# Kernel optimization log

Hardware: AMD Instinct MI355X
Metric: run time of the kernel (lower is better)

## Reference

```python
import jax, jax.numpy as jnp
import numpy as np

B, N, D, DK = 8, 2048, 1024, 64
GAMMA = 0.001

def setup_inputs() -> dict:
    key = jax.random.key(0)
    ks = jax.random.split(key, 6)
    x = jax.random.normal(ks[0], (B, N, D), dtype=jnp.float32)
    # nn.Linear weights are [out_features, in_features]; init std=gamma,
    # except fc1/fc2 (modules 4,5) which get std=1e-12 in the original.
    Wq = GAMMA * jax.random.normal(ks[1], (DK, D), dtype=jnp.float32)
    Wk = GAMMA * jax.random.normal(ks[2], (DK, D), dtype=jnp.float32)
    Wv = GAMMA * jax.random.normal(ks[3], (D, D), dtype=jnp.float32)
    W1 = 1e-12 * jax.random.normal(ks[4], (DK, D), dtype=jnp.float32)
    W2 = 1e-12 * jax.random.normal(ks[5], (D, DK), dtype=jnp.float32)
    return {"x": x, "Wq": Wq, "Wk": Wk, "Wv": Wv, "W1": W1, "W2": W2}

def reference(x, Wq, Wk, Wv, W1, W2):
    # Q,K: [B,N,DK]; V: [B,N,D]
    Q = jnp.einsum('bnd,kd->bnk', x, Wq)
    K = jnp.einsum('bnd,kd->bnk', x, Wk)
    V = jnp.einsum('bnd,ed->bne', x, Wv)
    # Linear (non-softmax) attention: (Q @ K^T) @ V
    scores = jnp.einsum('bnk,bmk->bnm', Q, K)      # [B,N,N]
    attention = jnp.einsum('bnm,bme->bne', scores, V)  # [B,N,D]
    x_skip = x + attention
    fc = jnp.einsum('bnd,kd->bnk', x_skip, W1)     # [B,N,DK]
    out = jnp.einsum('bnk,dk->bnd', fc, W2)        # [B,N,D]
    return out
```

## Files before the change

kernel.cpp:

```cpp
#include <hip/hip_runtime.h>

typedef __attribute__((ext_vector_type(8))) __bf16 bf16x8;
typedef __attribute__((ext_vector_type(4))) float f32x4;
typedef unsigned short u16;

#define MFMA16(a, b, c) __builtin_amdgcn_mfma_f32_16x16x32_bf16(a, b, c, 0, 0, 0)

__device__ __forceinline__ u16 f2bf(float f) {
    unsigned u = __float_as_uint(f);
    unsigned r = ((u >> 16) & 1u) + 0x7fffu;
    return (u16)((u + r) >> 16);
}
__device__ __forceinline__ float bf2f(u16 h) {
    return __uint_as_float(((unsigned)h) << 16);
}
__device__ __forceinline__ bf16x8 frag(const u16* base, int rtile, int lane, int kofs) {
    return *(const bf16x8*)(base + (rtile + (lane & 15)) * 72 + kofs + (lane >> 4) * 8);
}

__global__ __launch_bounds__(256) void qkf_kernel(
    const float* __restrict__ x, const float* __restrict__ Wq,
    const float* __restrict__ Wk, const float* __restrict__ W1,
    float* __restrict__ Qp, float* __restrict__ Kp, float* __restrict__ fcp)
{
    __shared__ __align__(16) u16 SM[6 * 4608];
    u16* Xh  = SM;
    u16* Xl  = SM + 4608;
    u16* Wqh = SM + 2 * 4608;
    u16* Wkh = SM + 3 * 4608;
    u16* W1h = SM + 4 * 4608;
    u16* W1l = SM + 5 * 4608;

    const int tid  = threadIdx.x;
    const int lane = tid & 63;
    const int wv   = tid >> 6;
    const int r0   = wv * 16;
    const long row0 = (long)blockIdx.x * 64;
    const int kb   = blockIdx.y * 512;
    const long sOf = (long)blockIdx.y * 1048576;

    const f32x4 zero = {0.f, 0.f, 0.f, 0.f};
    f32x4 qa[4], ka[4], fa[4];
#pragma unroll
    for (int i = 0; i < 4; ++i) { qa[i] = zero; ka[i] = zero; fa[i] = zero; }

    const int sr = tid >> 4;
    const int sk = (tid & 15) * 4;

    float4 xv[4], qv[4], kv[4], w1v[4];
#define QKF_LOAD(K0)                                                          \
    {                                                                         \
        _Pragma("unroll")                                                     \
        for (int i = 0; i < 4; ++i) {                                         \
            int r = sr + i * 16;                                              \
            xv[i]  = *(const float4*)(x  + (row0 + r) * 1024 + (K0) + sk);    \
            qv[i]  = *(const float4*)(Wq + (long)r * 1024 + (K0) + sk);       \
            kv[i]  = *(const float4*)(Wk + (long)r * 1024 + (K0) + sk);       \
            w1v[i] = *(const float4*)(W1 + (long)r * 1024 + (K0) + sk);       \
        }                                                                     \
    }

    QKF_LOAD(kb)
    for (int ch = 0; ch < 8; ++ch) {
        if (ch) __syncthreads();
#pragma unroll
        for (int i = 0; i < 4; ++i) {
            int r = sr + i * 16;
            ushort4 h, l;
            h.x = f2bf(xv[i].x); l.x = f2bf(xv[i].x - bf2f(h.x));
            h.y = f2bf(xv[i].y); l.y = f2bf(xv[i].y - bf2f(h.y));
            h.z = f2bf(xv[i].z); l.z = f2bf(xv[i].z - bf2f(h.z));
            h.w = f2bf(xv[i].w); l.w = f2bf(xv[i].w - bf2f(h.w));
            *(ushort4*)&Xh[r * 72 + sk] = h;
            *(ushort4*)&Xl[r * 72 + sk] = l;
            ushort4 hq;
            hq.x = f2bf(qv[i].x); hq.y = f2bf(qv[i].y);
            hq.z = f2bf(qv[i].z); hq.w = f2bf(qv[i].w);
            *(ushort4*)&Wqh[r * 72 + sk] = hq;
            ushort4 hk;
            hk.x = f2bf(kv[i].x); hk.y = f2bf(kv[i].y);
            hk.z = f2bf(kv[i].z); hk.w = f2bf(kv[i].w);
            *(ushort4*)&Wkh[r * 72 + sk] = hk;
            ushort4 hw, lw;
            hw.x = f2bf(w1v[i].x); lw.x = f2bf(w1v[i].x - bf2f(hw.x));
            hw.y = f2bf(w1v[i].y); lw.y = f2bf(w1v[i].y - bf2f(hw.y));
            hw.z = f2bf(w1v[i].z); lw.z = f2bf(w1v[i].z - bf2f(hw.z));
            hw.w = f2bf(w1v[i].w); lw.w = f2bf(w1v[i].w - bf2f(hw.w));
            *(ushort4*)&W1h[r * 72 + sk] = hw;
            *(ushort4*)&W1l[r * 72 + sk] = lw;
        }
        __syncthreads();
        if (ch < 7) QKF_LOAD(kb + (ch + 1) * 64)
#pragma unroll
        for (int kk = 0; kk < 64; kk += 32) {
            bf16x8 ah = frag(Xh, r0, lane, kk);
            bf16x8 al = frag(Xl, r0, lane, kk);
#pragma unroll
            for (int ct = 0; ct < 4; ++ct) {
                qa[ct] = MFMA16(ah, frag(Wqh, ct * 16, lane, kk), qa[ct]);
                ka[ct] = MFMA16(ah, frag(Wkh, ct * 16, lane, kk), ka[ct]);
                bf16x8 bh = frag(W1h, ct * 16, lane, kk);
                fa[ct] = MFMA16(ah, bh, fa[ct]);
                fa[ct] = MFMA16(al, bh, fa[ct]);
                fa[ct] = MFMA16(ah, frag(W1l, ct * 16, lane, kk), fa[ct]);
            }
        }
    }
#undef QKF_LOAD

    const int rr = r0 + (lane >> 4) * 4;
    const int cc = lane & 15;
#pragma unroll
    for (int ct = 0; ct < 4; ++ct)
#pragma unroll
        for (int g = 0; g < 4; ++g) {
            long o = sOf + (row0 + rr + g) * 64 + ct * 16 + cc;
            Qp[o]  = qa[ct][g];
            Kp[o]  = ka[ct][g];
            fcp[o] = fa[ct][g];
        }
}

__global__ __launch_bounds__(256) void s_kernel(
    const float* __restrict__ Kp, const float* __restrict__ x,
    float* __restrict__ Sp)
{
    __shared__ __align__(16) u16 Kt[64 * 72];
    __shared__ __align__(16) u16 Xt[64 * 72];

    const int tid = threadIdx.x, lane = tid & 63, wv = tid >> 6;
    const int dt = blockIdx.x, ks = blockIdx.y, b = blockIdx.z;
    const int n0 = ks * 256, d0 = dt * 64;

    const float* Kq = Kp + ((long)b * 2048 + n0) * 64;
    const float* xp = x  + ((long)b * 2048 + n0) * 1024 + d0;

    const f32x4 zero = {0.f, 0.f, 0.f, 0.f};
    f32x4 acc[4];
#pragma unroll
    for (int i = 0; i < 4; ++i) acc[i] = zero;

    float4 kf[4], xv[4];
#define SK_LOAD(NB)                                                           \
    {                                                                         \
        _Pragma("unroll")                                                     \
        for (int i = 0; i < 4; ++i) {                                         \
            float4 a = *(const float4*)(Kq + (long)((NB) + lane) * 64 + wv * 16 + i * 4); \
            float4 c = *(const float4*)(Kq + 1048576 + (long)((NB) + lane) * 64 + wv * 16 + i * 4); \
            kf[i].x = a.x + c.x; kf[i].y = a.y + c.y;                         \
            kf[i].z = a.z + c.z; kf[i].w = a.w + c.w;                         \
            xv[i] = *(const float4*)(xp + (long)((NB) + lane) * 1024 + wv * 16 + i * 4); \
        }                                                                     \
    }

    SK_LOAD(0)
    for (int ch = 0; ch < 4; ++ch) {
        if (ch) __syncthreads();
#pragma unroll
        for (int i = 0; i < 4; ++i) {
            Kt[(wv * 16 + i * 4 + 0) * 72 + lane] = f2bf(kf[i].x);
            Kt[(wv * 16 + i * 4 + 1) * 72 + lane] = f2bf(kf[i].y);
            Kt[(wv * 16 + i * 4 + 2) * 72 + lane] = f2bf(kf[i].z);
            Kt[(wv * 16 + i * 4 + 3) * 72 + lane] = f2bf(kf[i].w);
            Xt[(wv * 16 + i * 4 + 0) * 72 + lane] = f2bf(xv[i].x);
            Xt[(wv * 16 + i * 4 + 1) * 72 + lane] = f2bf(xv[i].y);
            Xt[(wv * 16 + i * 4 + 2) * 72 + lane] = f2bf(xv[i].z);
            Xt[(wv * 16 + i * 4 + 3) * 72 + lane] = f2bf(xv[i].w);
        }
        __syncthreads();
        if (ch < 3) SK_LOAD((ch + 1) * 64)
#pragma unroll
        for (int kk = 0; kk < 64; kk += 32) {
            bf16x8 a = frag(Kt, wv * 16, lane, kk);
#pragma unroll
            for (int ct = 0; ct < 4; ++ct)
                acc[ct] = MFMA16(a, frag(Xt, ct * 16, lane, kk), acc[ct]);
        }
    }
#undef SK_LOAD

    float* C = Sp + ((long)ks * 8 + b) * 65536 + d0;
    const int rr = wv * 16 + (lane >> 4) * 4;
    const int cc = lane & 15;
#pragma unroll
    for (int ct = 0; ct < 4; ++ct)
#pragma unroll
        for (int g = 0; g < 4; ++g)
            C[(long)(rr + g) * 1024 + ct * 16 + cc] = acc[ct][g];
}

template <int AMODE, int BMODE, bool SPLIT, int ASLAB, int BSLAB, int CSLAB>
__global__ __launch_bounds__(256) void mm_nt(
    const void* __restrict__ Ap, int lda, long bsA, long slabA,
    const void* __restrict__ Bp, int ldb, long bsB, long slabB,
    float* __restrict__ Cp, int ldc, long bsC, long splitC,
    const float* __restrict__ Cin, long slabCin,
    int Kred, int nksplit)
{
    __shared__ __align__(16) u16 SMEM[(SPLIT ? 4 : 2) * 4608];
    u16* Ah = SMEM;
    u16* Bh = SMEM + 4608;
    u16* Al = SPLIT ? SMEM + 2 * 4608 : nullptr;
    u16* Bl = SPLIT ? SMEM + 3 * 4608 : nullptr;

    const int tid = threadIdx.x, lane = tid & 63, wv = tid >> 6;
    const int bm = blockIdx.x, bn = blockIdx.y;
    const int batch = blockIdx.z / nksplit;
    const int ks = blockIdx.z % nksplit;
    const int Kper = Kred / nksplit;
    const long kOff = (long)ks * Kper;

    const int r4 = tid >> 4, k4 = (tid & 15) * 4;
    const int r8 = tid >> 3, k8 = (tid & 7) * 8;

    const f32x4 zero = {0.f, 0.f, 0.f, 0.f};
    f32x4 acc[4];
#pragma unroll
    for (int i = 0; i < 4; ++i) acc[i] = zero;

    float4 fva[4], fvb[4];
    uint4  uva[2], uvb[2];
    float  tvb[16];

#define MM_LOADA(K0)                                                          \
    if constexpr (AMODE == 0) {                                               \
        const float* A = (const float*)Ap + (long)batch * bsA                 \
                       + (long)bm * 64 * lda + (K0);                          \
        _Pragma("unroll")                                                     \
        for (int i = 0; i < 4; ++i) {                                         \
            const float* p = A + (long)(r4 + i * 16) * lda + k4;              \
            float4 v = *(const float4*)p;                                     \
            _Pragma("unroll")                                                 \
            for (int s = 1; s < ASLAB; ++s) {                                 \
                float4 w = *(const float4*)(p + (long)s * slabA);             \
                v.x += w.x; v.y += w.y; v.z += w.z; v.w += w.w;               \
            }                                                                 \
            fva[i] = v;                                                       \
        }                                                                     \
    } else {                                                                  \
        const u16* A = (const u16*)Ap + (long)batch * bsA                     \
                     + (long)bm * 64 * lda + (K0);                            \
        _Pragma("unroll")                                                     \
        for (int i = 0; i < 2; ++i)                                           \
            uva[i] = *(const uint4*)(A + (long)(r8 + i * 32) * lda + k8);     \
    }
#define MM_LOADB(K0)                                                          \
    if constexpr (BMODE == 0) {                                               \
        const float* Bq = (const float*)Bp + (long)batch * bsB                \
                        + (long)bn * 64 * ldb + (K0);                         \
        _Pragma("unroll")                                                     \
        for (int i = 0; i < 4; ++i) {                                         \
            const float* p = Bq + (long)(r4 + i * 16) * ldb + k4;             \
            float4 v = *(const float4*)p;                                     \
            _Pragma("unroll")                                                 \
            for (int s = 1; s < BSLAB; ++s) {                                 \
                float4 w = *(const float4*)(p + (long)s * slabB);             \
                v.x += w.x; v.y += w.y; v.z += w.z; v.w += w.w;               \
            }                                                                 \
            fvb[i] = v;                                                       \
        }                                                                     \
    } else if constexpr (BMODE == 1) {                                        \
        const u16* Bq = (const u16*)Bp + (long)batch * bsB                    \
                      + (long)bn * 64 * ldb + (K0);                           \
        _Pragma("unroll")                                                     \
        for (int i = 0; i < 2; ++i)                                           \
            uvb[i] = *(const uint4*)(Bq + (long)(r8 + i * 32) * ldb + k8);    \
    } else {                                                                  \
        const float* Bq = (const float*)Bp + (long)batch * bsB                \
                        + (long)(K0) * ldb + (long)bn * 64;                   \
        _Pragma("unroll")                                                     \
        for (int i = 0; i < 16; ++i)                                          \
            tvb[i] = Bq[(long)((tid >> 6) + i * 4) * ldb + (tid & 63)];       \
    }

    MM_LOADA(kOff) MM_LOADB(kOff)
    for (int k0 = 0; k0 < Kper; k0 += 64) {
        if (k0) __syncthreads();
        if constexpr (AMODE == 0) {
#pragma unroll
            for (int i = 0; i < 4; ++i) {
                int r = r4 + i * 16;
                ushort4 h;
                h.x = f2bf(fva[i].x); h.y = f2bf(fva[i].y);
                h.z = f2bf(fva[i].z); h.w = f2bf(fva[i].w);
                *(ushort4*)&Ah[r * 72 + k4] = h;
                if constexpr (SPLIT) {
                    ushort4 l;
                    l.x = f2bf(fva[i].x - bf2f(h.x)); l.y = f2bf(fva[i].y - bf2f(h.y));
                    l.z = f2bf(fva[i].z - bf2f(h.z)); l.w = f2bf(fva[i].w - bf2f(h.w));
                    *(ushort4*)&Al[r * 72 + k4] = l;
                }
            }
        } else {
#pragma unroll
            for (int i = 0; i < 2; ++i)
                *(uint4*)&Ah[(r8 + i * 32) * 72 + k8] = uva[i];
        }
        if constexpr (BMODE == 0) {
#pragma unroll
            for (int i = 0; i < 4; ++i) {
                int r = r4 + i * 16;
                ushort4 h;
                h.x = f2bf(fvb[i].x); h.y = f2bf(fvb[i].y);
                h.z = f2bf(fvb[i].z); h.w = f2bf(fvb[i].w);
                *(ushort4*)&Bh[r * 72 + k4] = h;
                if constexpr (SPLIT) {
                    ushort4 l;
                    l.x = f2bf(fvb[i].x - bf2f(h.x)); l.y = f2bf(fvb[i].y - bf2f(h.y));
                    l.z = f2bf(fvb[i].z - bf2f(h.z)); l.w = f2bf(fvb[i].w - bf2f(h.w));
                    *(ushort4*)&Bl[r * 72 + k4] = l;
                }
            }
        } else if constexpr (BMODE == 1) {
#pragma unroll
            for (int i = 0; i < 2; ++i)
                *(uint4*)&Bh[(r8 + i * 32) * 72 + k8] = uvb[i];
        } else {
#pragma unroll
            for (int i = 0; i < 16; ++i)
                Bh[(tid & 63) * 72 + (tid >> 6) + i * 4] = f2bf(tvb[i]);
        }
        __syncthreads();
        if (k0 + 64 < Kper) { MM_LOADA(kOff + k0 + 64) MM_LOADB(kOff + k0 + 64) }
#pragma unroll
        for (int kk = 0; kk < 64; kk += 32) {
            bf16x8 ah = frag(Ah, wv * 16, lane, kk);
            bf16x8 al;
            if constexpr (SPLIT) al = frag(Al, wv * 16, lane, kk);
#pragma unroll
            for (int ct = 0; ct < 4; ++ct) {
                bf16x8 bh = frag(Bh, ct * 16, lane, kk);
                acc[ct] = MFMA16(ah, bh, acc[ct]);
                if constexpr (SPLIT) {
                    acc[ct] = MFMA16(al, bh, acc[ct]);
                    acc[ct] = MFMA16(ah, frag(Bl, ct * 16, lane, kk), acc[ct]);
                }
            }
        }
    }
#undef MM_LOADA
#undef MM_LOADB

    const long coff = (long)batch * bsC + (long)bm * 64 * ldc + (long)bn * 64;
    float* C = Cp + coff + (long)ks * splitC;
    const int rr = wv * 16 + (lane >> 4) * 4;
    const int cc = lane & 15;
#pragma unroll
    for (int ct = 0; ct < 4; ++ct)
#pragma unroll
        for (int g = 0; g < 4; ++g) {
            long idx = (long)(rr + g) * ldc + ct * 16 + cc;
            float v = acc[ct][g];
            if constexpr (CSLAB > 0) {
                const float* Ci = Cin + coff + idx;
#pragma unroll
                for (int s = 0; s < CSLAB; ++s) v += Ci[(long)s * slabCin];
            }
            C[idx] = v;
        }
}

extern "C" void kernel_launch(void* const* d_in, const int* in_sizes, int n_in,
                              void* d_out, int out_size, void* d_ws, size_t ws_size,
                              hipStream_t stream)
{
    const float* x  = (const float*)d_in[0];
    const float* Wq = (const float*)d_in[1];
    const float* Wk = (const float*)d_in[2];
    const float* Wv = (const float*)d_in[3];
    const float* W1 = (const float*)d_in[4];
    const float* W2 = (const float*)d_in[5];
    float* out = (float*)d_out;

    const size_t QPB = 8388608, KPB = 8388608, FCPB = 8388608,
                 SPB = 16777216, GPB = 2097152, PBB = 2097152, FCB = 4194304;
    const size_t need = QPB + KPB + FCPB + SPB + GPB + PBB + FCB;

    float *Qp, *Kp, *fcp, *Sp, *Gp, *PBp, *fcb;
    if (ws_size >= need) {
        char* w = (char*)d_ws;
        Qp  = (float*)w;  w += QPB;
        Kp  = (float*)w;  w += KPB;
        fcp = (float*)w;  w += FCPB;
        Sp  = (float*)w;  w += SPB;
        Gp  = (float*)w;  w += GPB;
        PBp = (float*)w;  w += PBB;
        fcb = (float*)w;
    } else {
        char* o = (char*)d_out;
        Qp  = (float*)o;  o += QPB;
        Kp  = (float*)o;  o += KPB;
        fcp = (float*)o;  o += FCPB;
        Sp  = (float*)o;  o += SPB;
        Gp  = (float*)o;  o += GPB;
        PBp = (float*)o;
        fcb = (float*)d_ws;
    }

    qkf_kernel<<<dim3(256, 2), 256, 0, stream>>>(x, Wq, Wk, W1, Qp, Kp, fcp);

    s_kernel<<<dim3(16, 8, 8), 256, 0, stream>>>(Kp, x, Sp);

    mm_nt<0, 2, false, 1, 1, 0><<<dim3(1, 16, 8), 256, 0, stream>>>(
        W1, 1024, 0, 0,   Wv, 1024, 0, 0,
        Gp, 1024, 0, 65536L, nullptr, 0, 1024, 8);

    mm_nt<0, 0, false, 8, 8, 0><<<dim3(1, 1, 128), 256, 0, stream>>>(
        Gp, 1024, 0, 65536L,   Sp, 1024, 65536L, 524288L,
        PBp, 64, 4096L, 32768L, nullptr, 0, 1024, 16);

    mm_nt<0, 0, false, 2, 16, 2><<<dim3(32, 1, 8), 256, 0, stream>>>(
        Qp, 64, 131072L, 1048576L,   PBp, 64, 4096L, 32768L,
        fcb, 64, 131072L, 0, fcp, 1048576L, 64, 1);

    mm_nt<0, 0, true, 1, 1, 0><<<dim3(256, 16, 1), 256, 0, stream>>>(
        fcb, 64, 0, 0,   W2, 64, 0, 0,
        out, 1024, 0, 0, nullptr, 0, 64, 1);
}
```

Before: 207.0 us.

## Split qkf K-reduction four ways and fuse final two matmuls into one kernel

The QK/fc projection kernel now splits the D reduction into four slabs of 256 with a 32-wide K chunk. That doubles the grid and shrinks shared memory so more blocks can be resident, with a launch-bounds occupancy hint added. The last two matmuls (Q·PB plus fc residual, then the fc·W2 output projection) are fused into a single fcout kernel. It sums the split-K partials on load and keeps the fc tile in shared memory, avoiding an intermediate global buffer and a launch. The trade-off is larger partial buffers and more partial-sum reads in the downstream kernels. The mm_nt template is also trimmed of its unused modes.

```diff
diff --git a/kernel.cpp b/kernel.cpp
--- a/kernel.cpp
+++ b/kernel.cpp
@@ -17,46 +17,50 @@
 __device__ __forceinline__ bf16x8 frag(const u16* base, int rtile, int lane, int kofs) {
     return *(const bf16x8*)(base + (rtile + (lane & 15)) * 72 + kofs + (lane >> 4) * 8);
 }
-
-__global__ __launch_bounds__(256) void qkf_kernel(
+__device__ __forceinline__ bf16x8 frag40(const u16* base, int rtile, int lane) {
+    return *(const bf16x8*)(base + (rtile + (lane & 15)) * 40 + (lane >> 4) * 8);
+}
+
+__global__ __launch_bounds__(256, 4) void qkf_kernel(
     const float* __restrict__ x, const float* __restrict__ Wq,
     const float* __restrict__ Wk, const float* __restrict__ W1,
     float* __restrict__ Qp, float* __restrict__ Kp, float* __restrict__ fcp)
 {
-    __shared__ __align__(16) u16 SM[6 * 4608];
+    __shared__ __align__(16) u16 SM[6 * 2560];
     u16* Xh  = SM;
-    u16* Xl  = SM + 4608;
-    u16* Wqh = SM + 2 * 4608;
-    u16* Wkh = SM + 3 * 4608;
-    u16* W1h = SM + 4 * 4608;
-    u16* W1l = SM + 5 * 4608;
+    u16* Xl  = SM + 2560;
+    u16* Wqh = SM + 2 * 2560;
+    u16* Wkh = SM + 3 * 2560;
+    u16* W1h = SM + 4 * 2560;
+    u16* W1l = SM + 5 * 2560;
 
     const int tid  = threadIdx.x;
     const int lane = tid & 63;
     const int wv   = tid >> 6;
     const int r0   = wv * 16;
     const long row0 = (long)blockIdx.x * 64;
-    const int kb   = blockIdx.y * 512;
-    const long sOf = (long)blockIdx.y * 1048576;
+    const int ks   = blockIdx.y;
+    const int kb   = ks * 256;
+    const long sOf = (long)ks * 1048576;
 
     const f32x4 zero = {0.f, 0.f, 0.f, 0.f};
     f32x4 qa[4], ka[4], fa[4];
 #pragma unroll
     for (int i = 0; i < 4; ++i) { qa[i] = zero; ka[i] = zero; fa[i] = zero; }
 
-    const int sr = tid >> 4;
-    const int sk = (tid & 15) * 4;
-
-    float4 xv[4], qv[4], kv[4], w1v[4];
+    const int sr  = tid >> 2;
+    const int skq = (tid & 3) * 8;
+
+    float4 xv[2], qv[2], kv[2], w1v[2];
 #define QKF_LOAD(K0)                                                          \
     {                                                                         \
         _Pragma("unroll")                                                     \
-        for (int i = 0; i < 4; ++i) {                                         \
-            int r = sr + i * 16;                                              \
-            xv[i]  = *(const float4*)(x  + (row0 + r) * 1024 + (K0) + sk);    \
-            qv[i]  = *(const float4*)(Wq + (long)r * 1024 + (K0) + sk);       \
-            kv[i]  = *(const float4*)(Wk + (long)r * 1024 + (K0) + sk);       \
-            w1v[i] = *(const float4*)(W1 + (long)r * 1024 + (K0) + sk);       \
+        for (int h = 0; h < 2; ++h) {                                         \
+            int col = (K0) + skq + h * 4;                                     \
+            xv[h]  = *(const float4*)(x  + (row0 + sr) * 1024 + col);         \
+            qv[h]  = *(const float4*)(Wq + (long)sr * 1024 + col);            \
+            kv[h]  = *(const float4*)(Wk + (long)sr * 1024 + col);            \
+            w1v[h] = *(const float4*)(W1 + (long)sr * 1024 + col);            \
         }                                                                     \
     }
 
@@ -64,45 +68,44 @@
     for (int ch = 0; ch < 8; ++ch) {
         if (ch) __syncthreads();
 #pragma unroll
-        for (int i = 0; i < 4; ++i) {
-            int r = sr + i * 16;
-            ushort4 h, l;
-            h.x = f2bf(xv[i].x); l.x = f2bf(xv[i].x - bf2f(h.x));
-            h.y = f2bf(xv[i].y); l.y = f2bf(xv[i].y - bf2f(h.y));
-            h.z = f2bf(xv[i].z); l.z = f2bf(xv[i].z - bf2f(h.z));
-            h.w = f2bf(xv[i].w); l.w = f2bf(xv[i].w - bf2f(h.w));
-            *(ushort4*)&Xh[r * 72 + sk] = h;
-            *(ushort4*)&Xl[r * 72 + sk] = l;
+        for (int h = 0; h < 2; ++h) {
+            int o = sr * 40 + skq + h * 4;
+            ushort4 hx, lx;
+            hx.x = f2bf(xv[h].x); lx.x = f2bf(xv[h].x - bf2f(hx.x));
+            hx.y = f2bf(xv[h].y); lx.y = f2bf(xv[h].y - bf2f(hx.y));
+            hx.z = f2bf(xv[h].z); lx.z = f2bf(xv[h].z - bf2f(hx.z));
+            hx.w = f2bf(xv[h].w); lx.w = f2bf(xv[h].w - bf2f(hx.w));
+            *(ushort4*)&Xh[o] = hx;
+            *(ushort4*)&Xl[o] = lx;
             ushort4 hq;
-            hq.x = f2bf(qv[i].x); hq.y = f2bf(qv[i].y);
-            hq.z = f2bf(qv[i].z); hq.w = f2bf(qv[i].w);
-            *(ushort4*)&Wqh[r * 72 + sk] = hq;
+            hq.x = f2bf(qv[h].x); hq.y = f2bf(qv[h].y);
+            hq.z = f2bf(qv[h].z); hq.w = f2bf(qv[h].w);
+            *(ushort4*)&Wqh[o] = hq;
             ushort4 hk;
-            hk.x = f2bf(kv[i].x); hk.y = f2bf(kv[i].y);
-            hk.z = f2bf(kv[i].z); hk.w = f2bf(kv[i].w);
-            *(ushort4*)&Wkh[r * 72 + sk] = hk;
+            hk.x = f2bf(kv[h].x); hk.y = f2bf(kv[h].y);
+            hk.z = f2bf(kv[h].z); hk.w = f2bf(kv[h].w);
+            *(ushort4*)&Wkh[o] = hk;
             ushort4 hw, lw;
-            hw.x = f2bf(w1v[i].x); lw.x = f2bf(w1v[i].x - bf2f(hw.x));
-            hw.y = f2bf(w1v[i].y); lw.y = f2bf(w1v[i].y - bf2f(hw.y));
-            hw.z = f2bf(w1v[i].z); lw.z = f2bf(w1v[i].z - bf2f(hw.z));
-            hw.w = f2bf(w1v[i].w); lw.w = f2bf(w1v[i].w - bf2f(hw.w));
-            *(ushort4*)&W1h[r * 72 + sk] = hw;
-            *(ushort4*)&W1l[r * 72 + sk] = lw;
+            hw.x = f2bf(w1v[h].x); lw.x = f2bf(w1v[h].x - bf2f(hw.x));
+            hw.y = f2bf(w1v[h].y); lw.y = f2bf(w1v[h].y - bf2f(hw.y));
+            hw.z = f2bf(w1v[h].z); lw.z = f2bf(w1v[h].z - bf2f(hw.z));
+            hw.w = f2bf(w1v[h].w); lw.w = f2bf(w1v[h].w - bf2f(hw.w));
+            *(ushort4*)&W1h[o] = hw;
+            *(ushort4*)&W1l[o] = lw;
         }
         __syncthreads();
-        if (ch < 7) QKF_LOAD(kb + (ch + 1) * 64)
-#pragma unroll
-        for (int kk = 0; kk < 64; kk += 32) {
-            bf16x8 ah = frag(Xh, r0, lane, kk);
-            bf16x8 al = frag(Xl, r0, lane, kk);
+        if (ch < 7) QKF_LOAD(kb + (ch + 1) * 32)
+        {
+            bf16x8 ah = frag40(Xh, r0, lane);
+            bf16x8 al = frag40(Xl, r0, lane);
 #pragma unroll
             for (int ct = 0; ct < 4; ++ct) {
-                qa[ct] = MFMA16(ah, frag(Wqh, ct * 16, lane, kk), qa[ct]);
-                ka[ct] = MFMA16(ah, frag(Wkh, ct * 16, lane, kk), ka[ct]);
-                bf16x8 bh = frag(W1h, ct * 16, lane, kk);
+                qa[ct] = MFMA16(ah, frag40(Wqh, ct * 16, lane), qa[ct]);
+                ka[ct] = MFMA16(ah, frag40(Wkh, ct * 16, lane), ka[ct]);
+                bf16x8 bh = frag40(W1h, ct * 16, lane);
                 fa[ct] = MFMA16(ah, bh, fa[ct]);
                 fa[ct] = MFMA16(al, bh, fa[ct]);
-                fa[ct] = MFMA16(ah, frag(W1l, ct * 16, lane, kk), fa[ct]);
+                fa[ct] = MFMA16(ah, frag40(W1l, ct * 16, lane), fa[ct]);
             }
         }
     }
@@ -121,7 +124,7 @@
         }
 }
 
-__global__ __launch_bounds__(256) void s_kernel(
+__global__ __launch_bounds__(256, 4) void s_kernel(
     const float* __restrict__ Kp, const float* __restrict__ x,
     float* __restrict__ Sp)
 {
@@ -145,10 +148,14 @@
     {                                                                         \
         _Pragma("unroll")                                                     \
         for (int i = 0; i < 4; ++i) {                                         \
-            float4 a = *(const float4*)(Kq + (long)((NB) + lane) * 64 + wv * 16 + i * 4); \
-            float4 c = *(const float4*)(Kq + 1048576 + (long)((NB) + lane) * 64 + wv * 16 + i * 4); \
-            kf[i].x = a.x + c.x; kf[i].y = a.y + c.y;                         \
-            kf[i].z = a.z + c.z; kf[i].w = a.w + c.w;                         \
+            const float* kp0 = Kq + (long)((NB) + lane) * 64 + wv * 16 + i * 4; \
+            float4 a = *(const float4*)kp0;                                   \
+            _Pragma("unroll")                                                 \
+            for (int s = 1; s < 4; ++s) {                                     \
+                float4 c = *(const float4*)(kp0 + (long)s * 1048576);         \
+                a.x += c.x; a.y += c.y; a.z += c.z; a.w += c.w;               \
+            }                                                                 \
+            kf[i] = a;                                                        \
             xv[i] = *(const float4*)(xp + (long)((NB) + lane) * 1024 + wv * 16 + i * 4); \
         }                                                                     \
     }
@@ -189,19 +196,16 @@
             C[(long)(rr + g) * 1024 + ct * 16 + cc] = acc[ct][g];
 }
 
-template <int AMODE, int BMODE, bool SPLIT, int ASLAB, int BSLAB, int CSLAB>
+template <int AMODE, int BMODE, int ASLAB, int BSLAB>
 __global__ __launch_bounds__(256) void mm_nt(
     const void* __restrict__ Ap, int lda, long bsA, long slabA,
     const void* __restrict__ Bp, int ldb, long bsB, long slabB,
     float* __restrict__ Cp, int ldc, long bsC, long splitC,
-    const float* __restrict__ Cin, long slabCin,
     int Kred, int nksplit)
 {
-    __shared__ __align__(16) u16 SMEM[(SPLIT ? 4 : 2) * 4608];
+    __shared__ __align__(16) u16 SMEM[2 * 4608];
     u16* Ah = SMEM;
     u16* Bh = SMEM + 4608;
-    u16* Al = SPLIT ? SMEM + 2 * 4608 : nullptr;
-    u16* Bl = SPLIT ? SMEM + 3 * 4608 : nullptr;
 
     const int tid = threadIdx.x, lane = tid & 63, wv = tid >> 6;
     const int bm = blockIdx.x, bn = blockIdx.y;
@@ -211,7 +215,6 @@
     const long kOff = (long)ks * Kper;
 
     const int r4 = tid >> 4, k4 = (tid & 15) * 4;
-    const int r8 = tid >> 3, k8 = (tid & 7) * 8;
 
     const f32x4 zero = {0.f, 0.f, 0.f, 0.f};
     f32x4 acc[4];
@@ -219,11 +222,10 @@
     for (int i = 0; i < 4; ++i) acc[i] = zero;
 
     float4 fva[4], fvb[4];
-    uint4  uva[2], uvb[2];
     float  tvb[16];
 
 #define MM_LOADA(K0)                                                          \
-    if constexpr (AMODE == 0) {                                               \
+    {                                                                         \
         const float* A = (const float*)Ap + (long)batch * bsA                 \
                        + (long)bm * 64 * lda + (K0);                          \
         _Pragma("unroll")                                                     \
@@ -237,12 +239,6 @@
             }                                                                 \
             fva[i] = v;                                                       \
         }                                                                     \
-    } else {                                                                  \
-        const u16* A = (const u16*)Ap + (long)batch * bsA                     \
-                     + (long)bm * 64 * lda + (K0);                            \
-        _Pragma("unroll")                                                     \
-        for (int i = 0; i < 2; ++i)                                           \
-            uva[i] = *(const uint4*)(A + (long)(r8 + i * 32) * lda + k8);     \
     }
 #define MM_LOADB(K0)                                                          \
     if constexpr (BMODE == 0) {                                               \
@@ -259,12 +255,6 @@
             }                                                                 \
             fvb[i] = v;                                                       \
         }                                                                     \
-    } else if constexpr (BMODE == 1) {                                        \
-        const u16* Bq = (const u16*)Bp + (long)batch * bsB                    \
-                      + (long)bn * 64 * ldb + (K0);                           \
-        _Pragma("unroll")                                                     \
-        for (int i = 0; i < 2; ++i)                                           \
-            uvb[i] = *(const uint4*)(Bq + (long)(r8 + i * 32) * ldb + k8);    \
     } else {                                                                  \
         const float* Bq = (const float*)Bp + (long)batch * bsB                \
                         + (long)(K0) * ldb + (long)bn * 64;                   \
@@ -276,25 +266,13 @@
     MM_LOADA(kOff) MM_LOADB(kOff)
     for (int k0 = 0; k0 < Kper; k0 += 64) {
         if (k0) __syncthreads();
-        if constexpr (AMODE == 0) {
-#pragma unroll
-            for (int i = 0; i < 4; ++i) {
-                int r = r4 + i * 16;
-                ushort4 h;
-                h.x = f2bf(fva[i].x); h.y = f2bf(fva[i].y);
-                h.z = f2bf(fva[i].z); h.w = f2bf(fva[i].w);
-                *(ushort4*)&Ah[r * 72 + k4] = h;
-                if constexpr (SPLIT) {
-                    ushort4 l;
-                    l.x = f2bf(fva[i].x - bf2f(h.x)); l.y = f2bf(fva[i].y - bf2f(h.y));
-                    l.z = f2bf(fva[i].z - bf2f(h.z)); l.w = f2bf(fva[i].w - bf2f(h.w));
-                    *(ushort4*)&Al[r * 72 + k4] = l;
-                }
-            }
-        } else {
-#pragma unroll
-            for (int i = 0; i < 2; ++i)
-                *(uint4*)&Ah[(r8 + i * 32) * 72 + k8] = uva[i];
+#pragma unroll
+        for (int i = 0; i < 4; ++i) {
+            int r = r4 + i * 16;
+            ushort4 h;
+            h.x = f2bf(fva[i].x); h.y = f2bf(fva[i].y);
+            h.z = f2bf(fva[i].z); h.w = f2bf(fva[i].w);
+            *(ushort4*)&Ah[r * 72 + k4] = h;
         }
         if constexpr (BMODE == 0) {
 #pragma unroll
@@ -304,17 +282,7 @@
                 h.x = f2bf(fvb[i].x); h.y = f2bf(fvb[i].y);
                 h.z = f2bf(fvb[i].z); h.w = f2bf(fvb[i].w);
                 *(ushort4*)&Bh[r * 72 + k4] = h;
-                if constexpr (SPLIT) {
-                    ushort4 l;
-                    l.x = f2bf(fvb[i].x - bf2f(h.x)); l.y = f2bf(fvb[i].y - bf2f(h.y));
-                    l.z = f2bf(fvb[i].z - bf2f(h.z)); l.w = f2bf(fvb[i].w - bf2f(h.w));
-                    *(ushort4*)&Bl[r * 72 + k4] = l;
-                }
             }
-        } else if constexpr (BMODE == 1) {
-#pragma unroll
-            for (int i = 0; i < 2; ++i)
-                *(uint4*)&Bh[(r8 + i * 32) * 72 + k8] = uvb[i];
         } else {
 #pragma unroll
             for (int i = 0; i < 16; ++i)
@@ -325,39 +293,141 @@
 #pragma unroll
         for (int kk = 0; kk < 64; kk += 32) {
             bf16x8 ah = frag(Ah, wv * 16, lane, kk);
-            bf16x8 al;
-            if constexpr (SPLIT) al = frag(Al, wv * 16, lane, kk);
+#pragma unroll
+            for (int ct = 0; ct < 4; ++ct)
+                acc[ct] = MFMA16(ah, frag(Bh, ct * 16, lane, kk), acc[ct]);
+        }
+    }
+#undef MM_LOADA
+#undef MM_LOADB
+
+    float* C = Cp + (long)batch * bsC + (long)ks * splitC
+             + (long)bm * 64 * ldc + (long)bn * 64;
+    const int rr = wv * 16 + (lane >> 4) * 4;
+    const int cc = lane & 15;
+#pragma unroll
+    for (int ct = 0; ct < 4; ++ct)
+#pragma unroll
+        for (int g = 0; g < 4; ++g)
+            C[(long)(rr + g) * ldc + ct * 16 + cc] = acc[ct][g];
+}
+
+__global__ __launch_bounds__(256) void fcout_kernel(
+    const float* __restrict__ Qp, const float* __restrict__ PBp,
+    const float* __restrict__ fcp, const float* __restrict__ W2,
+    float* __restrict__ out)
+{
+    __shared__ __align__(16) u16 Ah[4608];
+    __shared__ __align__(16) u16 Al[4608];
+    __shared__ __align__(16) u16 Bh[4608];
+    __shared__ __align__(16) u16 Bl[4608];
+
+    const int tid = threadIdx.x, lane = tid & 63, wv = tid >> 6;
+    const long row0 = (long)blockIdx.x * 64;
+    const int b = (int)(row0 >> 11);
+    const int r4 = tid >> 2, c16 = (tid & 3) * 16;
+
+#pragma unroll
+    for (int h = 0; h < 4; ++h) {
+        const float* qp0 = Qp + (row0 + r4) * 64 + c16 + h * 4;
+        float4 v = *(const float4*)qp0;
+#pragma unroll
+        for (int s = 1; s < 4; ++s) {
+            float4 w = *(const float4*)(qp0 + (long)s * 1048576);
+            v.x += w.x; v.y += w.y; v.z += w.z; v.w += w.w;
+        }
+        ushort4 hh;
+        hh.x = f2bf(v.x); hh.y = f2bf(v.y); hh.z = f2bf(v.z); hh.w = f2bf(v.w);
+        *(ushort4*)&Ah[r4 * 72 + c16 + h * 4] = hh;
+    }
+    const float* pb = PBp + (long)b * 4096;
+#pragma unroll
+    for (int h = 0; h < 4; ++h) {
+        float4 v = {0.f, 0.f, 0.f, 0.f};
+#pragma unroll
+        for (int s = 0; s < 16; ++s) {
+            float4 w = *(const float4*)(pb + (long)s * 32768 + r4 * 64 + c16 + h * 4);
+            v.x += w.x; v.y += w.y; v.z += w.z; v.w += w.w;
+        }
+        ushort4 hh;
+        hh.x = f2bf(v.x); hh.y = f2bf(v.y); hh.z = f2bf(v.z); hh.w = f2bf(v.w);
+        *(ushort4*)&Bh[r4 * 72 + c16 + h * 4] = hh;
+    }
+    __syncthreads();
+
+    const f32x4 zero = {0.f, 0.f, 0.f, 0.f};
+    f32x4 facc[4];
+#pragma unroll
+    for (int i = 0; i < 4; ++i) facc[i] = zero;
+#pragma unroll
+    for (int kk = 0; kk < 64; kk += 32) {
+        bf16x8 ah = frag(Ah, wv * 16, lane, kk);
+#pragma unroll
+        for (int ct = 0; ct < 4; ++ct)
+            facc[ct] = MFMA16(ah, frag(Bh, ct * 16, lane, kk), facc[ct]);
+    }
+
+    const int rr = wv * 16 + (lane >> 4) * 4;
+    const int cc = lane & 15;
+    __syncthreads();
+#pragma unroll
+    for (int ct = 0; ct < 4; ++ct)
+#pragma unroll
+        for (int g = 0; g < 4; ++g) {
+            float v = facc[ct][g];
+            long o = (row0 + rr + g) * 64 + ct * 16 + cc;
+#pragma unroll
+            for (int s = 0; s < 4; ++s) v += fcp[o + (long)s * 1048576];
+            u16 h = f2bf(v);
+            Ah[(rr + g) * 72 + ct * 16 + cc] = h;
+            Al[(rr + g) * 72 + ct * 16 + cc] = f2bf(v - bf2f(h));
+        }
+    __syncthreads();
+
+    float4 w2v[4];
+#define W2_LOAD(E0)                                                           \
+    {                                                                         \
+        _Pragma("unroll")                                                     \
+        for (int h = 0; h < 4; ++h)                                           \
+            w2v[h] = *(const float4*)(W2 + (long)((E0) + r4) * 64 + c16 + h * 4); \
+    }
+    W2_LOAD(0)
+    for (int et = 0; et < 16; ++et) {
+        if (et) __syncthreads();
+#pragma unroll
+        for (int h = 0; h < 4; ++h) {
+            ushort4 hh, ll;
+            hh.x = f2bf(w2v[h].x); ll.x = f2bf(w2v[h].x - bf2f(hh.x));
+            hh.y = f2bf(w2v[h].y); ll.y = f2bf(w2v[h].y - bf2f(hh.y));
+            hh.z = f2bf(w2v[h].z); ll.z = f2bf(w2v[h].z - bf2f(hh.z));
+            hh.w = f2bf(w2v[h].w); ll.w = f2bf(w2v[h].w - bf2f(hh.w));
+            *(ushort4*)&Bh[r4 * 72 + c16 + h * 4] = hh;
+            *(ushort4*)&Bl[r4 * 72 + c16 + h * 4] = ll;
+        }
+        __syncthreads();
+        if (et < 15) W2_LOAD((et + 1) * 64)
+        f32x4 oacc[4];
+#pragma unroll
+        for (int i = 0; i < 4; ++i) oacc[i] = zero;
+#pragma unroll
+        for (int kk = 0; kk < 64; kk += 32) {
+            bf16x8 fh = frag(Ah, wv * 16, lane, kk);
+            bf16x8 fl = frag(Al, wv * 16, lane, kk);
 #pragma unroll
             for (int ct = 0; ct < 4; ++ct) {
                 bf16x8 bh = frag(Bh, ct * 16, lane, kk);
-                acc[ct] = MFMA16(ah, bh, acc[ct]);
-                if constexpr (SPLIT) {
-                    acc[ct] = MFMA16(al, bh, acc[ct]);
-                    acc[ct] = MFMA16(ah, frag(Bl, ct * 16, lane, kk), acc[ct]);
-                }
+                oacc[ct] = MFMA16(fh, bh, oacc[ct]);
+                oacc[ct] = MFMA16(fl, bh, oacc[ct]);
+                oacc[ct] = MFMA16(fh, frag(Bl, ct * 16, lane, kk), oacc[ct]);
             }
         }
-    }
-#undef MM_LOADA
-#undef MM_LOADB
-
-    const long coff = (long)batch * bsC + (long)bm * 64 * ldc + (long)bn * 64;
-    float* C = Cp + coff + (long)ks * splitC;
-    const int rr = wv * 16 + (lane >> 4) * 4;
-    const int cc = lane & 15;
-#pragma unroll
-    for (int ct = 0; ct < 4; ++ct)
-#pragma unroll
-        for (int g = 0; g < 4; ++g) {
-            long idx = (long)(rr + g) * ldc + ct * 16 + cc;
-            float v = acc[ct][g];
-            if constexpr (CSLAB > 0) {
-                const float* Ci = Cin + coff + idx;
-#pragma unroll
-                for (int s = 0; s < CSLAB; ++s) v += Ci[(long)s * slabCin];
-            }
-            C[idx] = v;
-        }
+#pragma unroll
+        for (int ct = 0; ct < 4; ++ct)
+#pragma unroll
+            for (int g = 0; g < 4; ++g)
+                out[(row0 + rr + g) * 1024 + et * 64 + ct * 16 + cc] = oacc[ct][g];
+    }
+#undef W2_LOAD
 }
 
 extern "C" void kernel_launch(void* const* d_in, const int* in_sizes, int n_in,
@@ -372,11 +442,11 @@
     const float* W2 = (const float*)d_in[5];
     float* out = (float*)d_out;
 
-    const size_t QPB = 8388608, KPB = 8388608, FCPB = 8388608,
-                 SPB = 16777216, GPB = 2097152, PBB = 2097152, FCB = 4194304;
-    const size_t need = QPB + KPB + FCPB + SPB + GPB + PBB + FCB;
-
-    float *Qp, *Kp, *fcp, *Sp, *Gp, *PBp, *fcb;
+    const size_t QPB = 16777216, KPB = 16777216, FCPB = 16777216,
+                 SPB = 16777216, GPB = 2097152, PBB = 2097152;
+    const size_t need = QPB + KPB + FCPB + SPB + GPB + PBB;
+
+    float *Qp, *Kp, *fcp, *Sp, *Gp, *PBp;
     if (ws_size >= need) {
         char* w = (char*)d_ws;
         Qp  = (float*)w;  w += QPB;
@@ -384,36 +454,29 @@
         fcp = (float*)w;  w += FCPB;
         Sp  = (float*)w;  w += SPB;
         Gp  = (float*)w;  w += GPB;
-        PBp = (float*)w;  w += PBB;
-        fcb = (float*)w;
+        PBp = (float*)w;
     } else {
+        char* w = (char*)d_ws;
+        Qp  = (float*)w;  w += QPB;
+        fcp = (float*)w;  w += FCPB;
+        PBp = (float*)w;
         char* o = (char*)d_out;
-        Qp  = (float*)o;  o += QPB;
         Kp  = (float*)o;  o += KPB;
-        fcp = (float*)o;  o += FCPB;
         Sp  = (float*)o;  o += SPB;
-        Gp  = (float*)o;  o += GPB;
-        PBp = (float*)o;
-        fcb = (float*)d_ws;
-    }
-
-    qkf_kernel<<<dim3(256, 2), 256, 0, stream>>>(x, Wq, Wk, W1, Qp, Kp, fcp);
+        Gp  = (float*)o;
+    }
+
+    qkf_kernel<<<dim3(256, 4), 256, 0, stream>>>(x, Wq, Wk, W1, Qp, Kp, fcp);
+
+    mm_nt<0, 2, 1, 1><<<dim3(1, 16, 8), 256, 0, stream>>>(
+        W1, 1024, 0, 0,   Wv, 1024, 0, 0,
+        Gp, 1024, 0, 65536L, 1024, 8);
 
     s_kernel<<<dim3(16, 8, 8), 256, 0, stream>>>(Kp, x, Sp);
 
-    mm_nt<0, 2, false, 1, 1, 0><<<dim3(1, 16, 8), 256, 0, stream>>>(
-        W1, 1024, 0, 0,   Wv, 1024, 0, 0,
-        Gp, 1024, 0, 65536L, nullptr, 0, 1024, 8);
-
-    mm_nt<0, 0, false, 8, 8, 0><<<dim3(1, 1, 128), 256, 0, stream>>>(
+    mm_nt<0, 0, 8, 8><<<dim3(1, 1, 128), 256, 0, stream>>>(
         Gp, 1024, 0, 65536L,   Sp, 1024, 65536L, 524288L,
-        PBp, 64, 4096L, 32768L, nullptr, 0, 1024, 16);
-
-    mm_nt<0, 0, false, 2, 16, 2><<<dim3(32, 1, 8), 256, 0, stream>>>(
-        Qp, 64, 131072L, 1048576L,   PBp, 64, 4096L, 32768L,
-        fcb, 64, 131072L, 0, fcp, 1048576L, 64, 1);
-
-    mm_nt<0, 0, true, 1, 1, 0><<<dim3(256, 16, 1), 256, 0, stream>>>(
-        fcb, 64, 0, 0,   W2, 64, 0, 0,
-        out, 1024, 0, 0, nullptr, 0, 64, 1);
-}
+        PBp, 64, 4096L, 32768L, 1024, 16);
+
+    fcout_kernel<<<dim3(256), 256, 0, stream>>>(Qp, PBp, fcp, W2, out);
+}
```

Result: slower. 244.4 us (+18.1%).
